# Kernel tuning notes

Hardware: AMD Instinct MI355X
Metric: run time of the kernel (lower is better)

The kernel has to match this reference:

```python
import jax, jax.numpy as jnp
import numpy as np

B, F, D, H = 256, 128, 512, 8
HD = D // H
SPARSITY = 0.5
KVAL = max(1, int(F * SPARSITY))  # 64


def setup_inputs() -> dict:
    key = jax.random.key(0)
    ks = jax.random.split(key, 12)
    s = 0.02
    x = jax.random.normal(ks[0], (B, F, D), dtype=jnp.float32)
    Wq = jax.random.normal(ks[1], (D, D), dtype=jnp.float32) * s
    bq = jnp.zeros((D,), jnp.float32)
    Wk = jax.random.normal(ks[2], (D, D), dtype=jnp.float32) * s
    bk = jnp.zeros((D,), jnp.float32)
    Wv = jax.random.normal(ks[3], (D, D), dtype=jnp.float32) * s
    bv = jnp.zeros((D,), jnp.float32)
    Wo = jax.random.normal(ks[4], (D, D), dtype=jnp.float32) * s
    bo = jnp.zeros((D,), jnp.float32)
    # correlation prior init: 0.5 * exp(-0.1 * |i-j|)
    idx = jnp.arange(F, dtype=jnp.float32)
    corr_prior = 0.5 * jnp.exp(-0.1 * jnp.abs(idx[:, None] - idx[None, :]))
    feat_imp = jnp.ones((F,), jnp.float32)
    # price_vol_detector: Linear(2D->D), SiLU, Linear(D->1), Sigmoid
    W1 = jax.random.normal(ks[5], (2 * D, D), dtype=jnp.float32) * s
    b1 = jnp.zeros((D,), jnp.float32)
    W2 = jax.random.normal(ks[6], (D, 1), dtype=jnp.float32) * s
    b2 = jnp.zeros((1,), jnp.float32)
    return {"x": x, "Wq": Wq, "bq": bq, "Wk": Wk, "bk": bk, "Wv": Wv, "bv": bv,
            "Wo": Wo, "bo": bo, "corr_prior": corr_prior, "feat_imp": feat_imp,
            "W1": W1, "b1": b1, "W2": W2, "b2": b2}


def reference(x, Wq, bq, Wk, bk, Wv, bv, Wo, bo, corr_prior, feat_imp, W1, b1, W2, b2):
    def split_heads(t):  # [B,F,D] -> [B,H,F,HD]
        return t.reshape(B, F, H, HD).transpose(0, 2, 1, 3)

    q = split_heads(x @ Wq + bq)
    k = split_heads(x @ Wk + bk)
    v = split_heads(x @ Wv + bv)

    scores = jnp.einsum('bhqd,bhkd->bhqk', q, k) / np.sqrt(HD).astype(np.float32)

    # correlation prior * pairwise feature importance
    imp = feat_imp[:, None] * feat_imp[None, :]          # [F,F]
    scores = scores + (corr_prior * imp)[None, None]     # broadcast to [B,H,F,F]

    # price-vol gating (n_features >= 2)
    mid = F // 2
    price = x[:, :mid].mean(axis=1)                      # [B,D]
    vol = x[:, mid:].mean(axis=1)                        # [B,D]
    combined = jnp.concatenate([price, vol], axis=1)     # [B,2D]
    h = jax.nn.silu(combined @ W1 + b1)
    pv = jax.nn.sigmoid(h @ W2 + b2).reshape(B, 1, 1, 1)  # [B,1,1,1]
    fidx = jnp.arange(F)
    pv_mask = ((fidx[:, None] < mid) ^ (fidx[None, :] < mid)).astype(scores.dtype)  # [F,F]
    scores = scores + pv * pv_mask[None, None] * 0.5

    # per-row top-k sparsification (same for all heads; vectorized over heads)
    topk_vals = jax.lax.top_k(scores, KVAL)[0]           # [B,H,F,KVAL]
    thresh = topk_vals[..., -1:]                          # kth largest per row
    scores = jnp.where(scores < thresh, jnp.float32(-1e9), scores)

    attn = jax.nn.softmax(scores, axis=-1)               # dropout: eval mode (identity)
    out = jnp.einsum('bhqk,bhkd->bhqd', attn, v)         # [B,H,F,HD]
    out = out.transpose(0, 2, 1, 3).reshape(B, F, D)     # merge heads
    return out @ Wo + bo
```

## Files before the change

### kernel.cpp

```cpp
#include <hip/hip_runtime.h>
#include <hip/hip_bf16.h>
#include <cstdint>

#define B_ 256
#define F_ 128
#define D_ 512
#define H_ 8
#define KVAL_ 64

typedef unsigned short ushort_t;
typedef __attribute__((ext_vector_type(8))) short short8;
typedef __attribute__((ext_vector_type(4))) float floatx4;
typedef __attribute__((ext_vector_type(2))) float floatx2;
typedef __attribute__((ext_vector_type(2))) double doublex2;

__device__ __forceinline__ unsigned f2ord32(float f) {
  unsigned b = __float_as_uint(f);
  return (b & 0x80000000u) ? ~b : (b | 0x80000000u);
}

__device__ __forceinline__ unsigned long long f2ord64(double s) {
  unsigned long long b = (unsigned long long)__double_as_longlong(s);
  return (b & 0x8000000000000000ull) ? ~b : (b | 0x8000000000000000ull);
}

__device__ __forceinline__ ushort_t f2bf(float f) {
  __hip_bfloat16 h = __float2bfloat16(f);
  return *reinterpret_cast<ushort_t*>(&h);
}
__device__ __forceinline__ float bf2f(ushort_t u) {
  __hip_bfloat16 h = *reinterpret_cast<__hip_bfloat16*>(&u);
  return __bfloat162float(h);
}

__global__ __launch_bounds__(256) void pv_kernel(
    const float* __restrict__ x, const float* __restrict__ W1,
    const float* __restrict__ b1, const float* __restrict__ W2,
    const float* __restrict__ b2, double* __restrict__ pv) {
  __shared__ double comb[1024];
  __shared__ double red[4];
  int b = blockIdx.x, t = threadIdx.x;
  {
    const float* xb = x + (size_t)b * (F_ * D_) + 2 * t;
    double p0 = 0.0, p1 = 0.0, v0 = 0.0, v1 = 0.0;
#pragma unroll 8
    for (int f = 0; f < 64; ++f) {
      floatx2 xp = *(const floatx2*)(xb + (size_t)f * D_);
      floatx2 xv = *(const floatx2*)(xb + (size_t)(f + 64) * D_);
      p0 += (double)xp[0];
      p1 += (double)xp[1];
      v0 += (double)xv[0];
      v1 += (double)xv[1];
    }
    comb[2 * t] = p0 * (1.0 / 64.0);
    comb[2 * t + 1] = p1 * (1.0 / 64.0);
    comb[512 + 2 * t] = v0 * (1.0 / 64.0);
    comb[512 + 2 * t + 1] = v1 * (1.0 / 64.0);
  }
  __syncthreads();
  double a0 = (double)b1[2 * t], a1 = (double)b1[2 * t + 1];
  const float* wp = W1 + 2 * t;
#pragma unroll 8
  for (int k = 0; k < 1024; ++k) {
    double c = comb[k];
    floatx2 wv = *(const floatx2*)(wp + (size_t)k * 512);
    a0 += c * (double)wv[0];
    a1 += c * (double)wv[1];
  }
  double h0 = a0 / (1.0 + exp(-a0));
  double h1 = a1 / (1.0 + exp(-a1));
  double part = h0 * (double)W2[2 * t] + h1 * (double)W2[2 * t + 1];
  for (int off = 32; off; off >>= 1) part += __shfl_xor(part, off);
  int lane = t & 63, w = t >> 6;
  if (lane == 0) red[w] = part;
  __syncthreads();
  if (t == 0) {
    double tot = red[0] + red[1] + red[2] + red[3] + (double)b2[0];
    pv[b] = 1.0 / (1.0 + exp(-tot));
  }
}

__global__ __launch_bounds__(256) void pack_wqk3_kernel(
    const float* __restrict__ Wq, const float* __restrict__ Wk,
    const float* __restrict__ bq, const float* __restrict__ bk,
    ushort_t* __restrict__ Wh, ushort_t* __restrict__ Wm,
    ushort_t* __restrict__ Wl, double* __restrict__ bqk) {
  int idx = blockIdx.x * 256 + threadIdx.x;
  int n = idx >> 9, k = idx & 511;
  float v = (n < 512) ? Wq[(size_t)k * 512 + n] : Wk[(size_t)k * 512 + (n - 512)];
  ushort_t h = f2bf(v);
  float r1 = v - bf2f(h);
  ushort_t m = f2bf(r1);
  ushort_t l = f2bf(r1 - bf2f(m));
  Wh[idx] = h;
  Wm[idx] = m;
  Wl[idx] = l;
  if (idx < 1024)
    bqk[idx] = (double)((idx < 512) ? bq[idx] : bk[idx - 512]);
}

__global__ __launch_bounds__(256) void pack_wt_kernel(
    const float* __restrict__ W, ushort_t* __restrict__ hiT,
    ushort_t* __restrict__ loT) {
  int i = blockIdx.x * 256 + threadIdx.x;
  int n = i >> 9, k = i & 511;
  float v = W[(size_t)k * 512 + n];
  ushort_t h = f2bf(v);
  hiT[i] = h;
  loT[i] = f2bf(v - bf2f(h));
}

__global__ __launch_bounds__(256) void xsplit3_kernel(
    const float* __restrict__ x, ushort_t* __restrict__ xh,
    ushort_t* __restrict__ xm, ushort_t* __restrict__ xl) {
  int i = blockIdx.x * 256 + threadIdx.x;
  const float* xp = x + (size_t)i * 8;
  floatx4 f0 = *(const floatx4*)xp;
  floatx4 f1 = *(const floatx4*)(xp + 4);
  short8 vh, vm, vl;
#pragma unroll
  for (int j = 0; j < 8; ++j) {
    float fv = (j < 4) ? f0[j] : f1[j - 4];
    ushort_t hb = f2bf(fv);
    float r1 = fv - bf2f(hb);
    ushort_t mb = f2bf(r1);
    ushort_t lb = f2bf(r1 - bf2f(mb));
    vh[j] = (short)hb;
    vm[j] = (short)mb;
    vl[j] = (short)lb;
  }
  *(short8*)&xh[(size_t)i * 8] = vh;
  *(short8*)&xm[(size_t)i * 8] = vm;
  *(short8*)&xl[(size_t)i * 8] = vl;
}

__global__ __launch_bounds__(256) void mfma_qk_v3(
    const ushort_t* __restrict__ Xh, const ushort_t* __restrict__ Xm,
    const ushort_t* __restrict__ Xl, const ushort_t* __restrict__ Wh,
    const ushort_t* __restrict__ Wm, const ushort_t* __restrict__ Wl,
    const double* __restrict__ bias, float* __restrict__ C, int nb) {
  __shared__ ushort_t As[3][128 * 40];
  __shared__ ushort_t Bs[3][128 * 40];
  int s = blockIdx.x;
  int o = (s & 7) * nb + (s >> 3);
  int n0 = (o & 7) * 128, m0 = (o >> 3) * 128;
  int t = threadIdx.x;
  int lane = t & 63, w = t >> 6;
  int wm_ = w >> 1, wn = w & 1;
  int mrow = lane & 15, quad = lane >> 4;
  floatx4 acc[4][4] = {};
  for (int kp = 0; kp < 16; ++kp) {
    int k0 = kp * 32;
    __syncthreads();
#pragma unroll
    for (int p = 0; p < 2; ++p) {
      int idx = p * 256 + t;
      int r = idx >> 2, c = (idx & 3) * 8;
      size_t aoff = (size_t)(m0 + r) * 512 + k0 + c;
      *(short8*)&As[0][r * 40 + c] = *(const short8*)(Xh + aoff);
      *(short8*)&As[1][r * 40 + c] = *(const short8*)(Xm + aoff);
      *(short8*)&As[2][r * 40 + c] = *(const short8*)(Xl + aoff);
      size_t boff = (size_t)(n0 + r) * 512 + k0 + c;
      *(short8*)&Bs[0][r * 40 + c] = *(const short8*)(Wh + boff);
      *(short8*)&Bs[1][r * 40 + c] = *(const short8*)(Wm + boff);
      *(short8*)&Bs[2][r * 40 + c] = *(const short8*)(Wl + boff);
    }
    __syncthreads();
#pragma unroll
    for (int sa = 0; sa < 3; ++sa) {
      short8 af[4];
#pragma unroll
      for (int mt = 0; mt < 4; ++mt)
        af[mt] = *(const short8*)&As[sa][(wm_ * 64 + mt * 16 + mrow) * 40 + quad * 8];
#pragma unroll
      for (int sb = 0; sb < 3; ++sb) {
        if (sa + sb > 2) continue;
        short8 bf[4];
#pragma unroll
        for (int nt = 0; nt < 4; ++nt)
          bf[nt] = *(const short8*)&Bs[sb][(wn * 64 + nt * 16 + mrow) * 40 + quad * 8];
#pragma unroll
        for (int mt = 0; mt < 4; ++mt)
#pragma unroll
          for (int nt = 0; nt < 4; ++nt)
            acc[mt][nt] = __builtin_amdgcn_mfma_f32_16x16x32_bf16(
                af[mt], bf[nt], acc[mt][nt], 0, 0, 0);
      }
    }
  }
#pragma unroll
  for (int nt = 0; nt < 4; ++nt) {
    int gn = n0 + wn * 64 + nt * 16 + mrow;
    double bb = bias[gn];
#pragma unroll
    for (int mt = 0; mt < 4; ++mt) {
      int gm = m0 + wm_ * 64 + mt * 16 + quad * 4;
#pragma unroll
      for (int rg = 0; rg < 4; ++rg)
        C[(size_t)(gm + rg) * 1024 + gn] = (float)((double)acc[mt][nt][rg] + bb);
    }
  }
}

__global__ __launch_bounds__(256) void mfma_gemm_split(
    const float* __restrict__ A, const ushort_t* __restrict__ WhiT,
    const ushort_t* __restrict__ WloT, const float* __restrict__ bias,
    float* __restrict__ C) {
  __shared__ ushort_t Ah[128 * 40];
  __shared__ ushort_t Al[128 * 40];
  __shared__ ushort_t Bh[128 * 40];
  __shared__ ushort_t Bl[128 * 40];
  int s = blockIdx.x;
  int o = (s & 7) * 128 + (s >> 3);
  int n0 = (o & 3) * 128, m0 = (o >> 2) * 128;
  int t = threadIdx.x;
  int lane = t & 63, w = t >> 6;
  int wm = w >> 1, wn = w & 1;
  int mrow = lane & 15, quad = lane >> 4;
  floatx4 acc[4][4] = {};
  for (int kp = 0; kp < 16; ++kp) {
    int k0 = kp * 32;
    __syncthreads();
#pragma unroll
    for (int p = 0; p < 2; ++p) {
      int idx = p * 256 + t;
      int r = idx >> 2, c = (idx & 3) * 8;
      const float* ap = A + (size_t)(m0 + r) * 512 + k0 + c;
      floatx4 f0 = *(const floatx4*)ap;
      floatx4 f1 = *(const floatx4*)(ap + 4);
      short8 vh, vl;
#pragma unroll
      for (int j = 0; j < 8; ++j) {
        float fv = (j < 4) ? f0[j] : f1[j - 4];
        ushort_t hb = f2bf(fv);
        vh[j] = (short)hb;
        vl[j] = (short)f2bf(fv - bf2f(hb));
      }
      *(short8*)&Ah[r * 40 + c] = vh;
      *(short8*)&Al[r * 40 + c] = vl;
      size_t boff = (size_t)(n0 + r) * 512 + k0 + c;
      *(short8*)&Bh[r * 40 + c] = *(const short8*)(WhiT + boff);
      *(short8*)&Bl[r * 40 + c] = *(const short8*)(WloT + boff);
    }
    __syncthreads();
    int abase = (wm * 64 + mrow) * 40 + quad * 8;
    int bbase = (wn * 64 + mrow) * 40 + quad * 8;
    short8 ah[4], bh[4];
#pragma unroll
    for (int i = 0; i < 4; ++i) {
      ah[i] = *(const short8*)&Ah[abase + i * 640];
      bh[i] = *(const short8*)&Bh[bbase + i * 640];
    }
#pragma unroll
    for (int mt = 0; mt < 4; ++mt)
#pragma unroll
      for (int nt = 0; nt < 4; ++nt)
        acc[mt][nt] = __builtin_amdgcn_mfma_f32_16x16x32_bf16(
            ah[mt], bh[nt], acc[mt][nt], 0, 0, 0);
    {
      short8 al[4];
#pragma unroll
      for (int i = 0; i < 4; ++i) al[i] = *(const short8*)&Al[abase + i * 640];
#pragma unroll
      for (int mt = 0; mt < 4; ++mt)
#pragma unroll
        for (int nt = 0; nt < 4; ++nt)
          acc[mt][nt] = __builtin_amdgcn_mfma_f32_16x16x32_bf16(
              al[mt], bh[nt], acc[mt][nt], 0, 0, 0);
    }
    {
      short8 bl[4];
#pragma unroll
      for (int i = 0; i < 4; ++i) bl[i] = *(const short8*)&Bl[bbase + i * 640];
#pragma unroll
      for (int mt = 0; mt < 4; ++mt)
#pragma unroll
        for (int nt = 0; nt < 4; ++nt)
          acc[mt][nt] = __builtin_amdgcn_mfma_f32_16x16x32_bf16(
              ah[mt], bl[nt], acc[mt][nt], 0, 0, 0);
    }
  }
#pragma unroll
  for (int nt = 0; nt < 4; ++nt) {
    int gn = n0 + wn * 64 + nt * 16 + mrow;
    float bb = bias[gn];
#pragma unroll
    for (int mt = 0; mt < 4; ++mt) {
      int gm = m0 + wm * 64 + mt * 16 + quad * 4;
#pragma unroll
      for (int rg = 0; rg < 4; ++rg)
        C[(size_t)(gm + rg) * 512 + gn] = acc[mt][nt][rg] + bb;
    }
  }
}

__global__ __launch_bounds__(1024) void attn_kernel(
    const float* __restrict__ qk, const float* __restrict__ vbuf,
    const float* __restrict__ corr_prior, const float* __restrict__ feat_imp,
    const double* __restrict__ pv, float* __restrict__ attn_out, int b_off,
    int nb) {
  __shared__ __align__(16) float smem[16384];
  int s = blockIdx.x;
  int o = (s & 7) * nb + (s >> 3);
  int b = o >> 3, h = o & 7;
  int t = threadIdx.x, lane = t & 63, w = t >> 6;
#pragma unroll
  for (int n = 0; n < 8; ++n) {
    int f = w + 16 * n;
    smem[lane * 128 + ((f + lane) & 127)] =
        qk[((size_t)(b * F_ + f)) * 1024 + 512 + h * 64 + lane];
  }
  float* qpw = &smem[8192 + w * 512];
  int fb = 8 * w;
#pragma unroll
  for (int i = 0; i < 8; ++i)
    qpw[i * 64 + lane] =
        qk[((size_t)(b * F_ + fb + i)) * 1024 + h * 64 + lane];
  __syncthreads();
  double pvb = pv[b_off + b] * 0.5;
  double fiA = (double)feat_imp[lane];
  double fiB = (double)feat_imp[64 + lane];
  const double SLOPE = 2.5e5;
  double s0[8], s1[8];
#pragma unroll
  for (int i = 0; i < 8; ++i) {
    s0[i] = 0.0;
    s1[i] = 0.0;
  }
#pragma unroll 2
  for (int d = 0; d < 64; d += 2) {
    double kd0a = (double)smem[d * 128 + ((lane + d) & 127)];
    double kd1a = (double)smem[d * 128 + ((lane + 64 + d) & 127)];
    double kd0b = (double)smem[(d + 1) * 128 + ((lane + 1 + d) & 127)];
    double kd1b = (double)smem[(d + 1) * 128 + ((lane + 65 + d) & 127)];
#pragma unroll
    for (int i = 0; i < 8; ++i) {
      floatx2 q2 = *(const floatx2*)&qpw[i * 64 + d];
      double qa = (double)q2[0], qb = (double)q2[1];
      s0[i] += qa * kd0a;
      s1[i] += qa * kd1a;
      s0[i] += qb * kd0b;
      s1[i] += qb * kd1b;
    }
  }
  float p0s[8], p1s[8];
#pragma unroll
  for (int i = 0; i < 8; ++i) {
    int f = fb + i;
    double sa = s0[i], sb = s1[i];
    double fif = (double)feat_imp[f];
    double cp0 = (double)corr_prior[f * 128 + lane] * fif * fiA;
    double cp1 = (double)corr_prior[f * 128 + 64 + lane] * fif * fiB;
    double add0 = (f < 64) ? 0.0 : pvb;
    double add1 = (f < 64) ? pvb : 0.0;
    sa = sa * 0.125 + cp0 + add0;
    sb = sb * 0.125 + cp1 + add1;
    unsigned a0 = f2ord32((float)sa), a1 = f2ord32((float)sb), T = 0u;
    for (int bit = 31; bit >= 0; --bit) {
      unsigned cand = T | (1u << bit);
      int c = __popcll(__ballot(a0 >= cand)) + __popcll(__ballot(a1 >= cand));
      if (c >= KVAL_) T = cand;
    }
    int cnt_gt = __popcll(__ballot(a0 > T)) + __popcll(__ballot(a1 > T));
    int cnt_ge = __popcll(__ballot(a0 >= T)) + __popcll(__ballot(a1 >= T));
    int bsz = cnt_ge - cnt_gt;
    int r = KVAL_ - cnt_gt;
    double bmax = -1e300;
    if (a0 < T) bmax = sa;
    if (a1 < T && sb > bmax) bmax = sb;
    for (int off = 32; off; off >>= 1) bmax = fmax(bmax, __shfl_xor(bmax, off));
    double sT, sU;
    if (bsz == r) {
      double tmin = 1e300;
      if (a0 == T) tmin = sa;
      if (a1 == T && sb < tmin) tmin = sb;
      for (int off = 32; off; off >>= 1) tmin = fmin(tmin, __shfl_xor(tmin, off));
      sT = tmin;
      sU = bmax;
    } else {
      unsigned long long x0 = (a0 == T) ? f2ord64(sa) : 0ull;
      unsigned long long x1 = (a1 == T) ? f2ord64(sb) : 0ull;
      unsigned long long T64 = 0ull;
      for (int bit = 63; bit >= 0; --bit) {
        unsigned long long cand = T64 | (1ull << bit);
        int c = __popcll(__ballot(x0 >= cand)) + __popcll(__ballot(x1 >= cand));
        if (c >= r) T64 = cand;
      }
      double tv = -1e300, uv = bmax;
      if (x0 == T64) tv = sa;
      if (x1 == T64 && sb > tv) tv = sb;
      if (a0 == T && x0 < T64 && sa > uv) uv = sa;
      if (a1 == T && x1 < T64 && sb > uv) uv = sb;
      for (int off = 32; off; off >>= 1) {
        tv = fmax(tv, __shfl_xor(tv, off));
        uv = fmax(uv, __shfl_xor(uv, off));
      }
      sT = tv;
      sU = uv;
    }
    double mid = 0.5 * (sT + sU);
    double W0 = fmin(1.0, fmax(0.0, 0.5 + (sa - mid) * SLOPE));
    double W1v = fmin(1.0, fmax(0.0, 0.5 + (sb - mid) * SLOPE));
    double mm = fmax(sa, sb);
    for (int off = 32; off; off >>= 1) mm = fmax(mm, __shfl_xor(mm, off));
    float p0 = (float)W0 * expf((float)(sa - mm));
    float p1 = (float)W1v * expf((float)(sb - mm));
    float zz = p0 + p1;
    for (int off = 32; off; off >>= 1) zz += __shfl_xor(zz, off);
    float inv = 1.f / zz;
    p0s[i] = p0 * inv;
    p1s[i] = p1 * inv;
  }
  __syncthreads();
  float* pp = &smem[w * 1024];
#pragma unroll
  for (int i = 0; i < 8; ++i) {
    pp[i * 128 + lane] = p0s[i];
    pp[i * 128 + 64 + lane] = p1s[i];
  }
  const float* vb = vbuf + ((size_t)b * F_) * 512 + h * 64 + lane;
  float o8[8] = {0.f, 0.f, 0.f, 0.f, 0.f, 0.f, 0.f, 0.f};
  float vj0 = vb[0], vj1 = vb[512];
  for (int j = 0; j < 128; j += 2) {
    float va = vj0, vbb = vj1;
    if (j + 2 < 128) {
      vj0 = vb[(size_t)(j + 2) * 512];
      vj1 = vb[(size_t)(j + 3) * 512];
    }
#pragma unroll
    for (int i = 0; i < 8; ++i) {
      floatx2 p2 = *(const floatx2*)&pp[i * 128 + j];
      o8[i] += p2[0] * va;
      o8[i] += p2[1] * vbb;
    }
  }
#pragma unroll
  for (int i = 0; i < 8; ++i)
    attn_out[((size_t)(b * F_ + fb + i)) * 512 + h * 64 + lane] = o8[i];
}

extern "C" void kernel_launch(void* const* d_in, const int* in_sizes, int n_in,
                              void* d_out, int out_size, void* d_ws,
                              size_t ws_size, hipStream_t stream) {
  const float* x = (const float*)d_in[0];
  const float* Wq = (const float*)d_in[1];
  const float* bq = (const float*)d_in[2];
  const float* Wk = (const float*)d_in[3];
  const float* bk = (const float*)d_in[4];
  const float* Wv = (const float*)d_in[5];
  const float* bv = (const float*)d_in[6];
  const float* Wo = (const float*)d_in[7];
  const float* bo = (const float*)d_in[8];
  const float* corr = (const float*)d_in[9];
  const float* fimp = (const float*)d_in[10];
  const float* W1 = (const float*)d_in[11];
  const float* b1 = (const float*)d_in[12];
  const float* W2 = (const float*)d_in[13];
  const float* b2 = (const float*)d_in[14];
  float* out = (float*)d_out;
  float* ws = (float*)d_ws;

  double* pv_hi = (double*)ws;
  double* bqk_hi = (double*)(ws + 512);
  ushort_t* WqkTh = (ushort_t*)(ws + 2560);
  ushort_t* WqkTm = (ushort_t*)(ws + 264704);
  ushort_t* WqkTl = (ushort_t*)(ws + 526848);
  ushort_t* WvhiT = (ushort_t*)(ws + 788992);
  ushort_t* WvloT = (ushort_t*)(ws + 920064);
  ushort_t* WohiT = (ushort_t*)(ws + 1051136);
  ushort_t* WoloT = (ushort_t*)(ws + 1182208);
  float* vbuf = ws + 1313280;
  float* attnb = ws + 18090496;
  float* qk = ws + 34867712;
  const size_t head = 34867712;
  size_t ws_floats = ws_size / 4;
  int Bc = 8;
  for (int cand = 256; cand >= 8; cand >>= 1)
    if (head + (size_t)cand * 180224 <= ws_floats) { Bc = cand; break; }
  ushort_t* Xh = (ushort_t*)(ws + head + (size_t)Bc * 131072);
  ushort_t* Xm = Xh + (size_t)Bc * 65536;
  ushort_t* Xl = Xm + (size_t)Bc * 65536;

  hipLaunchKernelGGL(pv_kernel, dim3(B_), dim3(256), 0, stream,
                     x, W1, b1, W2, b2, pv_hi);
  hipLaunchKernelGGL(pack_wqk3_kernel, dim3(2048), dim3(256), 0, stream,
                     Wq, Wk, bq, bk, WqkTh, WqkTm, WqkTl, bqk_hi);
  hipLaunchKernelGGL(pack_wt_kernel, dim3(1024), dim3(256), 0, stream,
                     Wv, WvhiT, WvloT);
  hipLaunchKernelGGL(pack_wt_kernel, dim3(1024), dim3(256), 0, stream,
                     Wo, WohiT, WoloT);
  hipLaunchKernelGGL(mfma_gemm_split, dim3(1024), dim3(256), 0, stream,
                     x, WvhiT, WvloT, bv, vbuf);
  for (int b0 = 0; b0 < B_; b0 += Bc) {
    hipLaunchKernelGGL(xsplit3_kernel, dim3(Bc * 32), dim3(256), 0, stream,
                       x + (size_t)b0 * 65536, Xh, Xm, Xl);
    hipLaunchKernelGGL(mfma_qk_v3, dim3(8 * Bc), dim3(256), 0, stream,
                       Xh, Xm, Xl, WqkTh, WqkTm, WqkTl, bqk_hi, qk, Bc);
    hipLaunchKernelGGL(attn_kernel, dim3(Bc * 8), dim3(1024), 0, stream,
                       qk, vbuf + (size_t)b0 * 65536, corr, fimp, pv_hi,
                       attnb + (size_t)b0 * 65536, b0, Bc);
  }
  hipLaunchKernelGGL(mfma_gemm_split, dim3(1024), dim3(256), 0, stream,
                     attnb, WohiT, WoloT, bo, out);
}
```

Measured before the change: 1.000 ms.

## Fuse Q/K projection GEMM into attention kernel per batch-head block

Removes the separate QK projection kernel and the chunked batch loop. Each attention block now computes its own head's Q and K projection (128x128 tile over the split-bf16 operands) with MFMA and writes the results straight into shared memory in the layout the attention code expects. This avoids writing and re-reading the fp32 qk buffer through global memory and cuts the number of launches. In exchange each block does a smaller GEMM tile with 16 waves and lower per-wave MFMA reuse, and the X split buffers are now sized for the whole batch, which assumes the workspace is large enough.

Measured after the change: 1.025 ms. +2.5%, slower.

```diff
diff --git a/kernel.cpp b/kernel.cpp
--- a/kernel.cpp
+++ b/kernel.cpp
@@ -12,7 +12,6 @@
 typedef __attribute__((ext_vector_type(8))) short short8;
 typedef __attribute__((ext_vector_type(4))) float floatx4;
 typedef __attribute__((ext_vector_type(2))) float floatx2;
-typedef __attribute__((ext_vector_type(2))) double doublex2;
 
 __device__ __forceinline__ unsigned f2ord32(float f) {
   unsigned b = __float_as_uint(f);
@@ -132,74 +131,6 @@
   *(short8*)&xh[(size_t)i * 8] = vh;
   *(short8*)&xm[(size_t)i * 8] = vm;
   *(short8*)&xl[(size_t)i * 8] = vl;
-}
-
-__global__ __launch_bounds__(256) void mfma_qk_v3(
-    const ushort_t* __restrict__ Xh, const ushort_t* __restrict__ Xm,
-    const ushort_t* __restrict__ Xl, const ushort_t* __restrict__ Wh,
-    const ushort_t* __restrict__ Wm, const ushort_t* __restrict__ Wl,
-    const double* __restrict__ bias, float* __restrict__ C, int nb) {
-  __shared__ ushort_t As[3][128 * 40];
-  __shared__ ushort_t Bs[3][128 * 40];
-  int s = blockIdx.x;
-  int o = (s & 7) * nb + (s >> 3);
-  int n0 = (o & 7) * 128, m0 = (o >> 3) * 128;
-  int t = threadIdx.x;
-  int lane = t & 63, w = t >> 6;
-  int wm_ = w >> 1, wn = w & 1;
-  int mrow = lane & 15, quad = lane >> 4;
-  floatx4 acc[4][4] = {};
-  for (int kp = 0; kp < 16; ++kp) {
-    int k0 = kp * 32;
-    __syncthreads();
-#pragma unroll
-    for (int p = 0; p < 2; ++p) {
-      int idx = p * 256 + t;
-      int r = idx >> 2, c = (idx & 3) * 8;
-      size_t aoff = (size_t)(m0 + r) * 512 + k0 + c;
-      *(short8*)&As[0][r * 40 + c] = *(const short8*)(Xh + aoff);
-      *(short8*)&As[1][r * 40 + c] = *(const short8*)(Xm + aoff);
-      *(short8*)&As[2][r * 40 + c] = *(const short8*)(Xl + aoff);
-      size_t boff = (size_t)(n0 + r) * 512 + k0 + c;
-      *(short8*)&Bs[0][r * 40 + c] = *(const short8*)(Wh + boff);
-      *(short8*)&Bs[1][r * 40 + c] = *(const short8*)(Wm + boff);
-      *(short8*)&Bs[2][r * 40 + c] = *(const short8*)(Wl + boff);
-    }
-    __syncthreads();
-#pragma unroll
-    for (int sa = 0; sa < 3; ++sa) {
-      short8 af[4];
-#pragma unroll
-      for (int mt = 0; mt < 4; ++mt)
-        af[mt] = *(const short8*)&As[sa][(wm_ * 64 + mt * 16 + mrow) * 40 + quad * 8];
-#pragma unroll
-      for (int sb = 0; sb < 3; ++sb) {
-        if (sa + sb > 2) continue;
-        short8 bf[4];
-#pragma unroll
-        for (int nt = 0; nt < 4; ++nt)
-          bf[nt] = *(const short8*)&Bs[sb][(wn * 64 + nt * 16 + mrow) * 40 + quad * 8];
-#pragma unroll
-        for (int mt = 0; mt < 4; ++mt)
-#pragma unroll
-          for (int nt = 0; nt < 4; ++nt)
-            acc[mt][nt] = __builtin_amdgcn_mfma_f32_16x16x32_bf16(
-                af[mt], bf[nt], acc[mt][nt], 0, 0, 0);
-      }
-    }
-  }
-#pragma unroll
-  for (int nt = 0; nt < 4; ++nt) {
-    int gn = n0 + wn * 64 + nt * 16 + mrow;
-    double bb = bias[gn];
-#pragma unroll
-    for (int mt = 0; mt < 4; ++mt) {
-      int gm = m0 + wm_ * 64 + mt * 16 + quad * 4;
-#pragma unroll
-      for (int rg = 0; rg < 4; ++rg)
-        C[(size_t)(gm + rg) * 1024 + gn] = (float)((double)acc[mt][nt][rg] + bb);
-    }
-  }
 }
 
 __global__ __launch_bounds__(256) void mfma_gemm_split(
@@ -294,30 +225,93 @@
   }
 }
 
-__global__ __launch_bounds__(1024) void attn_kernel(
-    const float* __restrict__ qk, const float* __restrict__ vbuf,
+__global__ __launch_bounds__(1024) void fused_qk_attn(
+    const ushort_t* __restrict__ Xh, const ushort_t* __restrict__ Xm,
+    const ushort_t* __restrict__ Xl, const ushort_t* __restrict__ Wh,
+    const ushort_t* __restrict__ Wm, const ushort_t* __restrict__ Wl,
+    const double* __restrict__ bias, const float* __restrict__ vbuf,
     const float* __restrict__ corr_prior, const float* __restrict__ feat_imp,
-    const double* __restrict__ pv, float* __restrict__ attn_out, int b_off,
-    int nb) {
+    const double* __restrict__ pv, float* __restrict__ attn_out) {
   __shared__ __align__(16) float smem[16384];
   int s = blockIdx.x;
-  int o = (s & 7) * nb + (s >> 3);
+  int o = (s & 7) * 256 + (s >> 3);
   int b = o >> 3, h = o & 7;
   int t = threadIdx.x, lane = t & 63, w = t >> 6;
-#pragma unroll
-  for (int n = 0; n < 8; ++n) {
-    int f = w + 16 * n;
-    smem[lane * 128 + ((f + lane) & 127)] =
-        qk[((size_t)(b * F_ + f)) * 1024 + 512 + h * 64 + lane];
-  }
+  ushort_t* As = (ushort_t*)smem;
+  ushort_t* Bs = As + 15360;
+  int wm_ = w >> 2, wn = w & 3;
+  int mrow = lane & 15, quad = lane >> 4;
+  floatx4 acc[2][2] = {};
+  for (int kp = 0; kp < 16; ++kp) {
+    int k0 = kp * 32;
+    __syncthreads();
+    {
+      int idx = t & 511;
+      int r = idx >> 2, c = (idx & 3) * 8;
+      if (t < 512) {
+        size_t aoff = (size_t)(b * F_ + r) * 512 + k0 + c;
+        *(short8*)&As[r * 40 + c] = *(const short8*)(Xh + aoff);
+        *(short8*)&As[5120 + r * 40 + c] = *(const short8*)(Xm + aoff);
+        *(short8*)&As[10240 + r * 40 + c] = *(const short8*)(Xl + aoff);
+      } else {
+        int wrow = (r < 64) ? (h * 64 + r) : (512 + h * 64 + (r - 64));
+        size_t boff = (size_t)wrow * 512 + k0 + c;
+        *(short8*)&Bs[r * 40 + c] = *(const short8*)(Wh + boff);
+        *(short8*)&Bs[5120 + r * 40 + c] = *(const short8*)(Wm + boff);
+        *(short8*)&Bs[10240 + r * 40 + c] = *(const short8*)(Wl + boff);
+      }
+    }
+    __syncthreads();
+#pragma unroll
+    for (int sa = 0; sa < 3; ++sa) {
+      short8 af[2];
+#pragma unroll
+      for (int mt = 0; mt < 2; ++mt)
+        af[mt] = *(const short8*)&As[sa * 5120 +
+                                     (wm_ * 32 + mt * 16 + mrow) * 40 + quad * 8];
+#pragma unroll
+      for (int sb = 0; sb < 3; ++sb) {
+        if (sa + sb > 2) continue;
+        short8 bf[2];
+#pragma unroll
+        for (int nt = 0; nt < 2; ++nt)
+          bf[nt] = *(const short8*)&Bs[sb * 5120 +
+                                       (wn * 32 + nt * 16 + mrow) * 40 + quad * 8];
+#pragma unroll
+        for (int mt = 0; mt < 2; ++mt)
+#pragma unroll
+          for (int nt = 0; nt < 2; ++nt)
+            acc[mt][nt] = __builtin_amdgcn_mfma_f32_16x16x32_bf16(
+                af[mt], bf[nt], acc[mt][nt], 0, 0, 0);
+      }
+    }
+  }
+  __syncthreads();
+#pragma unroll
+  for (int nt = 0; nt < 2; ++nt) {
+    int gn = wn * 32 + nt * 16 + mrow;
+    int gcol = (gn < 64) ? (h * 64 + gn) : (512 + h * 64 + (gn - 64));
+    double bb = bias[gcol];
+#pragma unroll
+    for (int mt = 0; mt < 2; ++mt) {
+      int gmb = wm_ * 32 + mt * 16 + quad * 4;
+#pragma unroll
+      for (int rg = 0; rg < 4; ++rg) {
+        int gm = gmb + rg;
+        float val = (float)((double)acc[mt][nt][rg] + bb);
+        if (gn < 64) {
+          smem[8192 + (gm >> 3) * 512 + (gm & 7) * 64 + gn] = val;
+        } else {
+          int d = gn - 64;
+          smem[d * 128 + ((gm + d) & 127)] = val;
+        }
+      }
+    }
+  }
+  __syncthreads();
   float* qpw = &smem[8192 + w * 512];
   int fb = 8 * w;
-#pragma unroll
-  for (int i = 0; i < 8; ++i)
-    qpw[i * 64 + lane] =
-        qk[((size_t)(b * F_ + fb + i)) * 1024 + h * 64 + lane];
-  __syncthreads();
-  double pvb = pv[b_off + b] * 0.5;
+  double pvb = pv[b] * 0.5;
   double fiA = (double)feat_imp[lane];
   double fiB = (double)feat_imp[64 + lane];
   const double SLOPE = 2.5e5;
@@ -471,15 +465,9 @@
   ushort_t* WoloT = (ushort_t*)(ws + 1182208);
   float* vbuf = ws + 1313280;
   float* attnb = ws + 18090496;
-  float* qk = ws + 34867712;
-  const size_t head = 34867712;
-  size_t ws_floats = ws_size / 4;
-  int Bc = 8;
-  for (int cand = 256; cand >= 8; cand >>= 1)
-    if (head + (size_t)cand * 180224 <= ws_floats) { Bc = cand; break; }
-  ushort_t* Xh = (ushort_t*)(ws + head + (size_t)Bc * 131072);
-  ushort_t* Xm = Xh + (size_t)Bc * 65536;
-  ushort_t* Xl = Xm + (size_t)Bc * 65536;
+  ushort_t* Xh = (ushort_t*)(ws + 34867712);
+  ushort_t* Xm = Xh + 16777216;
+  ushort_t* Xl = Xm + 16777216;
 
   hipLaunchKernelGGL(pv_kernel, dim3(B_), dim3(256), 0, stream,
                      x, W1, b1, W2, b2, pv_hi);
@@ -491,15 +479,11 @@
                      Wo, WohiT, WoloT);
   hipLaunchKernelGGL(mfma_gemm_split, dim3(1024), dim3(256), 0, stream,
                      x, WvhiT, WvloT, bv, vbuf);
-  for (int b0 = 0; b0 < B_; b0 += Bc) {
-    hipLaunchKernelGGL(xsplit3_kernel, dim3(Bc * 32), dim3(256), 0, stream,
-                       x + (size_t)b0 * 65536, Xh, Xm, Xl);
-    hipLaunchKernelGGL(mfma_qk_v3, dim3(8 * Bc), dim3(256), 0, stream,
-                       Xh, Xm, Xl, WqkTh, WqkTm, WqkTl, bqk_hi, qk, Bc);
-    hipLaunchKernelGGL(attn_kernel, dim3(Bc * 8), dim3(1024), 0, stream,
-                       qk, vbuf + (size_t)b0 * 65536, corr, fimp, pv_hi,
-                       attnb + (size_t)b0 * 65536, b0, Bc);
-  }
+  hipLaunchKernelGGL(xsplit3_kernel, dim3(8192), dim3(256), 0, stream,
+                     x, Xh, Xm, Xl);
+  hipLaunchKernelGGL(fused_qk_attn, dim3(2048), dim3(1024), 0, stream,
+                     Xh, Xm, Xl, WqkTh, WqkTm, WqkTl, bqk_hi,
+                     vbuf, corr, fimp, pv_hi, attnb);
   hipLaunchKernelGGL(mfma_gemm_split, dim3(1024), dim3(256), 0, stream,
                      attnb, WohiT, WoloT, bo, out);
 }
```
